# Performance work log

Measured on AMD Instinct MI355X. Metric: run time of the kernel, lower is better.

Reference implementation:

```python
import jax, jax.numpy as jnp
import numpy as np
import math

B, T, D, H, FF = 2, 2048, 1024, 16, 4096
DH = D // H
EPS = 1e-5

def _ternary(key, out_f, in_f):
    # TFLELayer: ternary-quantized linear weight in {-1,0,1} (stored as f32 here)
    return jax.random.randint(key, (out_f, in_f), -1, 2).astype(jnp.float32)

def setup_inputs() -> dict:
    key = jax.random.key(0)
    ks = jax.random.split(key, 8)
    x = jax.random.normal(ks[0], (B, T, D), dtype=jnp.float32)
    mask = jnp.triu(jnp.ones((T, T), dtype=bool), k=1)  # True = masked (causal)
    return {
        "x": x,
        "mask": mask,
        "ln1_g": jnp.ones((D,), jnp.float32), "ln1_b": jnp.zeros((D,), jnp.float32),
        "ln2_g": jnp.ones((D,), jnp.float32), "ln2_b": jnp.zeros((D,), jnp.float32),
        "Wq": _ternary(ks[1], D, D), "Wk": _ternary(ks[2], D, D),
        "Wv": _ternary(ks[3], D, D), "Wo": _ternary(ks[4], D, D),
        "Wff1": _ternary(ks[5], FF, D), "Wff2": _ternary(ks[6], D, FF),
    }

def _ln(x, g, b):
    mu = jnp.mean(x, axis=-1, keepdims=True)
    var = jnp.var(x, axis=-1, keepdims=True)
    return (x - mu) * jax.lax.rsqrt(var + EPS) * g + b

def reference(x, mask, ln1_g, ln1_b, ln2_g, ln2_b, Wq, Wk, Wv, Wo, Wff1, Wff2):
    h = _ln(x, ln1_g, ln1_b)
    q = (h @ Wq.T).reshape(B, T, H, DH).transpose(0, 2, 1, 3)  # (B,H,T,DH)
    k = (h @ Wk.T).reshape(B, T, H, DH).transpose(0, 2, 1, 3)
    v = (h @ Wv.T).reshape(B, T, H, DH).transpose(0, 2, 1, 3)
    scale = 1.0 / math.sqrt(DH)
    attn = jnp.einsum('bhqd,bhkd->bhqk', q, k) * scale
    attn = jnp.where(mask[None, None], -jnp.inf, attn)
    attn = jax.nn.softmax(attn, axis=-1)
    out = jnp.einsum('bhqk,bhkd->bhqd', attn, v)
    out = out.transpose(0, 2, 1, 3).reshape(B, T, D) @ Wo.T
    x = x + out
    h = _ln(x, ln2_g, ln2_b)
    ff = jax.nn.gelu(h @ Wff1.T, approximate=False)
    ff = ff @ Wff2.T
    return x + ff
```

## Files before the change

### kernel.cpp

```cpp
#include <hip/hip_runtime.h>

typedef __bf16 bf16;
typedef bf16 bf16x8 __attribute__((ext_vector_type(8)));
typedef bf16 bf16x4 __attribute__((ext_vector_type(4)));
typedef float f32x4 __attribute__((ext_vector_type(4)));

static __device__ __forceinline__ void async16(const void* g, void* l) {
  __builtin_amdgcn_global_load_lds((__attribute__((address_space(1))) void*)g,
                                   (__attribute__((address_space(3))) void*)l,
                                   16, 0, 0);
}

template <int N>
static __device__ __forceinline__ float ror16(float x) {
  const int y =
      __builtin_amdgcn_update_dpp(0, __float_as_int(x), 0x120 | N, 0xf, 0xf, true);
  return __int_as_float(y);
}
static __device__ __forceinline__ float rowmax16(float x) {
  x = fmaxf(x, ror16<8>(x));
  x = fmaxf(x, ror16<4>(x));
  x = fmaxf(x, ror16<2>(x));
  x = fmaxf(x, ror16<1>(x));
  return x;
}

__global__ __launch_bounds__(256) void ln1_cvt4(
    const float* __restrict__ x, const float* __restrict__ g,
    const float* __restrict__ b, bf16* __restrict__ hi, bf16* __restrict__ lo,
    const float* __restrict__ Wq, const float* __restrict__ Wk,
    const float* __restrict__ Wv, const float* __restrict__ Wo,
    bf16* __restrict__ wdst) {
  const int tid = threadIdx.x;
  if (blockIdx.x >= 4096) {
    const size_t i = ((size_t)(blockIdx.x - 4096) * 256 + tid) * 4;
    const size_t M1 = 1u << 20;
    const float* src = (i < M1) ? Wq : (i < 2 * M1) ? Wk : (i < 3 * M1) ? Wv : Wo;
    const size_t off = i & (M1 - 1);
    const float4 v = *(const float4*)(src + off);
    bf16x4 o = {(bf16)v.x, (bf16)v.y, (bf16)v.z, (bf16)v.w};
    *(bf16x4*)(wdst + i) = o;
    return;
  }
  const int row = blockIdx.x;
  const float* xr = x + (size_t)row * 1024;
  float v[4];
  float s1 = 0.f, s2 = 0.f;
#pragma unroll
  for (int j = 0; j < 4; ++j) {
    v[j] = xr[j * 256 + tid];
    s1 += v[j];
    s2 += v[j] * v[j];
  }
#pragma unroll
  for (int off = 1; off < 64; off <<= 1) {
    s1 += __shfl_xor(s1, off);
    s2 += __shfl_xor(s2, off);
  }
  __shared__ float ws1[4], ws2[4];
  const int wid = tid >> 6;
  if ((tid & 63) == 0) {
    ws1[wid] = s1;
    ws2[wid] = s2;
  }
  __syncthreads();
  s1 = ws1[0] + ws1[1] + ws1[2] + ws1[3];
  s2 = ws2[0] + ws2[1] + ws2[2] + ws2[3];
  const float mu = s1 * (1.f / 1024.f);
  const float var = s2 * (1.f / 1024.f) - mu * mu;
  const float rstd = 1.0f / sqrtf(var + 1e-5f);
#pragma unroll
  for (int j = 0; j < 4; ++j) {
    const int cc = j * 256 + tid;
    const float y = (v[j] - mu) * rstd * g[cc] + b[cc];
    const bf16 yh = (bf16)y;
    hi[(size_t)row * 1024 + cc] = yh;
    lo[(size_t)row * 1024 + cc] = (bf16)(y - (float)yh);
  }
}

__global__ __launch_bounds__(256) void ln_kernel(
    const float* __restrict__ x, const float* __restrict__ g,
    const float* __restrict__ b, bf16* __restrict__ hi) {
  const int row = blockIdx.x;
  const int tid = threadIdx.x;
  const float* xr = x + (size_t)row * 1024;
  float v[4];
  float s1 = 0.f, s2 = 0.f;
#pragma unroll
  for (int j = 0; j < 4; ++j) {
    v[j] = xr[j * 256 + tid];
    s1 += v[j];
    s2 += v[j] * v[j];
  }
#pragma unroll
  for (int off = 1; off < 64; off <<= 1) {
    s1 += __shfl_xor(s1, off);
    s2 += __shfl_xor(s2, off);
  }
  __shared__ float ws1[4], ws2[4];
  const int wid = tid >> 6;
  if ((tid & 63) == 0) {
    ws1[wid] = s1;
    ws2[wid] = s2;
  }
  __syncthreads();
  s1 = ws1[0] + ws1[1] + ws1[2] + ws1[3];
  s2 = ws2[0] + ws2[1] + ws2[2] + ws2[3];
  const float mu = s1 * (1.f / 1024.f);
  const float var = s2 * (1.f / 1024.f) - mu * mu;
  const float rstd = 1.0f / sqrtf(var + 1e-5f);
#pragma unroll
  for (int j = 0; j < 4; ++j) {
    const int cc = j * 256 + tid;
    const float y = (v[j] - mu) * rstd * g[cc] + b[cc];
    hi[(size_t)row * 1024 + cc] = (bf16)y;
  }
}

template <int EPI>
static __device__ __forceinline__ void gemm_body(
    const bf16* __restrict__ A, const bf16* __restrict__ B,
    void* __restrict__ Cv, const float* __restrict__ R, bf16* smem, int col0,
    int row0, int M, int N, int K) {
  bf16* sA0 = smem;
  bf16* sA1 = smem + 4096;
  bf16* sB0 = smem + 8192;
  bf16* sB1 = smem + 12288;
  const int tid = threadIdx.x;
  const int lane = tid & 63;
  const int wid = tid >> 6;
  const int wm = wid >> 1, wn = wid & 1;

  f32x4 acc[4][4];
  const f32x4 fzero = {0.f, 0.f, 0.f, 0.f};
#pragma unroll
  for (int i = 0; i < 4; ++i)
#pragma unroll
    for (int j = 0; j < 4; ++j) acc[i][j] = fzero;

  const int nk = K >> 6;
  const int r0 = tid >> 2, c0 = (tid & 3) << 3;
  const int r1 = (256 + tid) >> 2, c1 = ((256 + tid) & 3) << 3;
  const int wofs0 = (wid << 6) * 8;
  const int wofs1 = (256 + (wid << 6)) * 8;

  for (int kt = 0; kt < nk; ++kt) {
    const int k0 = kt << 6;
    async16(A + (size_t)(row0 + r0) * K + k0 + c0, sA0 + wofs0);
    async16(A + (size_t)(row0 + r1) * K + k0 + c1, sA0 + wofs1);
    async16(A + (size_t)(row0 + r0) * K + k0 + 32 + c0, sA1 + wofs0);
    async16(A + (size_t)(row0 + r1) * K + k0 + 32 + c1, sA1 + wofs1);
    async16(B + (size_t)(col0 + r0) * K + k0 + c0, sB0 + wofs0);
    async16(B + (size_t)(col0 + r1) * K + k0 + c1, sB0 + wofs1);
    async16(B + (size_t)(col0 + r0) * K + k0 + 32 + c0, sB1 + wofs0);
    async16(B + (size_t)(col0 + r1) * K + k0 + 32 + c1, sB1 + wofs1);
    __syncthreads();
    const int fr = lane & 15, fq = (lane >> 4) << 3;
#pragma unroll
    for (int t = 0; t < 2; ++t) {
      const bf16* sA = t ? sA1 : sA0;
      const bf16* sB = t ? sB1 : sB0;
      bf16x8 af[4], bfr[4];
#pragma unroll
      for (int i = 0; i < 4; ++i)
        af[i] = *(const bf16x8*)&sA[(wm * 64 + i * 16 + fr) * 32 + fq];
#pragma unroll
      for (int j = 0; j < 4; ++j)
        bfr[j] = *(const bf16x8*)&sB[(wn * 64 + j * 16 + fr) * 32 + fq];
#pragma unroll
      for (int i = 0; i < 4; ++i)
#pragma unroll
        for (int j = 0; j < 4; ++j)
          acc[i][j] = __builtin_amdgcn_mfma_f32_16x16x32_bf16(
              af[i], bfr[j], acc[i][j], 0, 0, 0);
    }
    __syncthreads();
  }

  const int fr = lane & 15, fq4 = (lane >> 4) << 2;
#pragma unroll
  for (int i = 0; i < 4; ++i) {
#pragma unroll
    for (int j = 0; j < 4; ++j) {
      const int rbase = row0 + wm * 64 + i * 16 + fq4;
      const int col = col0 + wn * 64 + j * 16 + fr;
      if constexpr (EPI == 5) {
        const int b = rbase >> 11, t = rbase & 2047;
        const int hh = col >> 6, d = col & 63;
        bf16x4 o4 = {(bf16)acc[i][j][0], (bf16)acc[i][j][1],
                     (bf16)acc[i][j][2], (bf16)acc[i][j][3]};
        *(bf16x4*)&((bf16*)Cv)[(((size_t)(b * 16 + hh)) * 64 + d) * 2048 + t] =
            o4;
      } else {
#pragma unroll
        for (int r = 0; r < 4; ++r) {
          const size_t idx = (size_t)(rbase + r) * N + col;
          const float val = acc[i][j][r];
          if constexpr (EPI == 0) {
            ((float*)Cv)[idx] = val;
          } else if constexpr (EPI == 2) {
            ((float*)Cv)[idx] = val + R[idx];
          } else {
            ((bf16*)Cv)[idx] =
                (bf16)(0.5f * val * (1.0f + erff(val * 0.7071067811865476f)));
          }
        }
      }
    }
  }
}

static __device__ __forceinline__ void gemm_split_merged(
    const bf16* __restrict__ A, const bf16* __restrict__ A2,
    const bf16* __restrict__ B, bf16* __restrict__ Chi, bf16* __restrict__ Clo,
    bf16* smem, float scale, int col0, int row0) {
  constexpr int K = 1024, N = 1024;
  bf16* sAh0 = smem;
  bf16* sAh1 = smem + 4096;
  bf16* sAl0 = smem + 8192;
  bf16* sAl1 = smem + 12288;
  bf16* sB0 = smem + 16384;
  bf16* sB1 = smem + 20480;
  const int tid = threadIdx.x;
  const int lane = tid & 63;
  const int wid = tid >> 6;
  const int wm = wid >> 1, wn = wid & 1;

  f32x4 acc[4][4];
  const f32x4 fzero = {0.f, 0.f, 0.f, 0.f};
#pragma unroll
  for (int i = 0; i < 4; ++i)
#pragma unroll
    for (int j = 0; j < 4; ++j) acc[i][j] = fzero;

  const int r0 = tid >> 2, c0 = (tid & 3) << 3;
  const int r1 = (256 + tid) >> 2, c1 = ((256 + tid) & 3) << 3;
  const int wofs0 = (wid << 6) * 8;
  const int wofs1 = (256 + (wid << 6)) * 8;

  for (int kt = 0; kt < 16; ++kt) {
    const int k0 = kt << 6;
    async16(A + (size_t)(row0 + r0) * K + k0 + c0, sAh0 + wofs0);
    async16(A + (size_t)(row0 + r1) * K + k0 + c1, sAh0 + wofs1);
    async16(A + (size_t)(row0 + r0) * K + k0 + 32 + c0, sAh1 + wofs0);
    async16(A + (size_t)(row0 + r1) * K + k0 + 32 + c1, sAh1 + wofs1);
    async16(A2 + (size_t)(row0 + r0) * K + k0 + c0, sAl0 + wofs0);
    async16(A2 + (size_t)(row0 + r1) * K + k0 + c1, sAl0 + wofs1);
    async16(A2 + (size_t)(row0 + r0) * K + k0 + 32 + c0, sAl1 + wofs0);
    async16(A2 + (size_t)(row0 + r1) * K + k0 + 32 + c1, sAl1 + wofs1);
    async16(B + (size_t)(col0 + r0) * K + k0 + c0, sB0 + wofs0);
    async16(B + (size_t)(col0 + r1) * K + k0 + c1, sB0 + wofs1);
    async16(B + (size_t)(col0 + r0) * K + k0 + 32 + c0, sB1 + wofs0);
    async16(B + (size_t)(col0 + r1) * K + k0 + 32 + c1, sB1 + wofs1);
    __syncthreads();
    const int fr = lane & 15, fq = (lane >> 4) << 3;
#pragma unroll
    for (int t = 0; t < 2; ++t) {
      const bf16* sAh = t ? sAh1 : sAh0;
      const bf16* sAl = t ? sAl1 : sAl0;
      const bf16* sB = t ? sB1 : sB0;
      bf16x8 ah[4], al[4], bfr[4];
#pragma unroll
      for (int i = 0; i < 4; ++i) {
        ah[i] = *(const bf16x8*)&sAh[(wm * 64 + i * 16 + fr) * 32 + fq];
        al[i] = *(const bf16x8*)&sAl[(wm * 64 + i * 16 + fr) * 32 + fq];
      }
#pragma unroll
      for (int j = 0; j < 4; ++j)
        bfr[j] = *(const bf16x8*)&sB[(wn * 64 + j * 16 + fr) * 32 + fq];
#pragma unroll
      for (int i = 0; i < 4; ++i)
#pragma unroll
        for (int j = 0; j < 4; ++j) {
          acc[i][j] = __builtin_amdgcn_mfma_f32_16x16x32_bf16(
              ah[i], bfr[j], acc[i][j], 0, 0, 0);
          acc[i][j] = __builtin_amdgcn_mfma_f32_16x16x32_bf16(
              al[i], bfr[j], acc[i][j], 0, 0, 0);
        }
    }
    __syncthreads();
  }

  const int fr = lane & 15, fq4 = (lane >> 4) << 2;
#pragma unroll
  for (int i = 0; i < 4; ++i)
#pragma unroll
    for (int j = 0; j < 4; ++j) {
      const int rbase = row0 + wm * 64 + i * 16 + fq4;
      const int col = col0 + wn * 64 + j * 16 + fr;
#pragma unroll
      for (int r = 0; r < 4; ++r) {
        const size_t idx = (size_t)(rbase + r) * N + col;
        const float vs = acc[i][j][r] * scale;
        const bf16 hi = (bf16)vs;
        Chi[idx] = hi;
        Clo[idx] = (bf16)(vs - (float)hi);
      }
    }
}

__global__ __launch_bounds__(256) void gemm_qkv(
    const bf16* __restrict__ A, const bf16* __restrict__ A2,
    const bf16* __restrict__ Bq, const bf16* __restrict__ Bk,
    const bf16* __restrict__ Bv, bf16* qh, bf16* ql, bf16* kh, bf16* kl,
    bf16* vt) {
  __shared__ bf16 smem[24576];
  const int which = blockIdx.x >> 3;
  const int col0 = (blockIdx.x & 7) * 128, row0 = blockIdx.y * 128;
  if (which == 2) {
    gemm_body<5>(A, Bv, (void*)vt, nullptr, smem, col0, row0, 4096, 1024,
                 1024);
  } else {
    gemm_split_merged(A, A2, which ? Bk : Bq, which ? kh : qh, which ? kl : ql,
                      smem, which ? 1.0f : 0.125f * 1.44269504088896f, col0,
                      row0);
  }
}

template <int EPI>
__global__ __launch_bounds__(256) void gemm_bt64(
    const bf16* __restrict__ A, const bf16* __restrict__ B,
    void* __restrict__ Cv, const float* __restrict__ R, int M, int N, int K) {
  __shared__ bf16 smem[24576];
  const int col0 = blockIdx.x * 64, row0 = blockIdx.y * 128;
  const int tid = threadIdx.x;
  const int lane = tid & 63;
  const int wid = tid >> 6;
  const int wm = wid >> 1, wn = wid & 1;

  f32x4 acc[4][2];
  const f32x4 fzero = {0.f, 0.f, 0.f, 0.f};
#pragma unroll
  for (int i = 0; i < 4; ++i)
#pragma unroll
    for (int j = 0; j < 2; ++j) acc[i][j] = fzero;

  const int nk = K >> 6;
  const int r0 = tid >> 2, c0 = (tid & 3) << 3;
  const int r1 = (256 + tid) >> 2, c1 = ((256 + tid) & 3) << 3;
  const int wofs0 = (wid << 6) * 8;
  const int wofs1 = (256 + (wid << 6)) * 8;

  auto stage = [&](int q, int kt) {
    const int k0 = kt << 6;
    bf16* base = smem + q * 12288;
    async16(A + (size_t)(row0 + r0) * K + k0 + c0, base + wofs0);
    async16(A + (size_t)(row0 + r1) * K + k0 + c1, base + wofs1);
    async16(A + (size_t)(row0 + r0) * K + k0 + 32 + c0, base + 4096 + wofs0);
    async16(A + (size_t)(row0 + r1) * K + k0 + 32 + c1, base + 4096 + wofs1);
    async16(B + (size_t)(col0 + r0) * K + k0 + c0, base + 8192 + wofs0);
    async16(B + (size_t)(col0 + r0) * K + k0 + 32 + c0, base + 10240 + wofs0);
  };

  stage(0, 0);
  __syncthreads();
  int cur = 0;
  for (int kt = 0; kt < nk; ++kt) {
    if (kt + 1 < nk) stage(cur ^ 1, kt + 1);
    const bf16* buf = smem + cur * 12288;
    const int fr = lane & 15, fq = (lane >> 4) << 3;
#pragma unroll
    for (int t = 0; t < 2; ++t) {
      const bf16* sA = buf + t * 4096;
      const bf16* sB = buf + 8192 + t * 2048;
      bf16x8 af[4], bfr[2];
#pragma unroll
      for (int i = 0; i < 4; ++i)
        af[i] = *(const bf16x8*)&sA[(wm * 64 + i * 16 + fr) * 32 + fq];
#pragma unroll
      for (int j = 0; j < 2; ++j)
        bfr[j] = *(const bf16x8*)&sB[(wn * 32 + j * 16 + fr) * 32 + fq];
#pragma unroll
      for (int i = 0; i < 4; ++i)
#pragma unroll
        for (int j = 0; j < 2; ++j)
          acc[i][j] = __builtin_amdgcn_mfma_f32_16x16x32_bf16(
              af[i], bfr[j], acc[i][j], 0, 0, 0);
    }
    __syncthreads();
    cur ^= 1;
  }

  const int fr = lane & 15, fq4 = (lane >> 4) << 2;
#pragma unroll
  for (int i = 0; i < 4; ++i) {
#pragma unroll
    for (int j = 0; j < 2; ++j) {
      const int rbase = row0 + wm * 64 + i * 16 + fq4;
      const int col = col0 + wn * 32 + j * 16 + fr;
#pragma unroll
      for (int r = 0; r < 4; ++r) {
        const size_t idx = (size_t)(rbase + r) * N + col;
        const float val = acc[i][j][r];
        if constexpr (EPI == 3) {
          ((bf16*)Cv)[idx] =
              (bf16)(0.5f * val * (1.0f + erff(val * 0.7071067811865476f)));
        } else if constexpr (EPI == 2) {
          ((float*)Cv)[idx] = val + R[idx];
        } else {
          ((float*)Cv)[idx] = val;
        }
      }
    }
  }
}

__global__ __launch_bounds__(256) void attn_cvt2(
    const bf16* __restrict__ qh_g, const bf16* __restrict__ ql_g,
    const bf16* __restrict__ kh_g, const bf16* __restrict__ kl_g,
    const bf16* __restrict__ vt_g, bf16* __restrict__ out,
    const float* __restrict__ Wf1, const float* __restrict__ Wf2,
    bf16* __restrict__ wdst) {
  __shared__ bf16 lds[18688];
  const int tid = threadIdx.x;
  if (blockIdx.x >= 1024) {
    const size_t i = ((size_t)(blockIdx.x - 1024) * 256 + tid) * 4;
    const size_t M4 = 4u << 20;
    const float* src = (i < M4) ? Wf1 : Wf2;
    const size_t off = (i < M4) ? i : i - M4;
    const float4 v = *(const float4*)(src + off);
    bf16x4 o4 = {(bf16)v.x, (bf16)v.y, (bf16)v.z, (bf16)v.w};
    *(bf16x4*)(wdst + i) = o4;
    return;
  }
  bf16* Kh = lds;
  bf16* Kl = lds + 4608;
  bf16* Vt = lds + 9216;
  bf16* Ps = lds + 13824;

  const int bid = blockIdx.x;
  const int u = bid & 255;
  const int s = bid >> 8;
  const int v = u >> 5;
  const int qbase = (3 - s) << 3;
  const int qt = qbase + ((s & 1) ? v : 7 - v);
  const int bh = (u & 7) * 4 + ((u >> 3) & 3);
  const int h = bh & 15;
  const int b = bh >> 4;
  const int t0 = qt << 6;
  const int w = tid >> 6;
  const int lane = tid & 63;
  const int c = lane & 15;
  const int quad = lane >> 4;

  const int r0 = tid >> 3, c0 = (tid & 7) << 3;
  const int r1 = (tid + 256) >> 3, c1 = ((tid + 256) & 7) << 3;

  const size_t qrow =
      ((size_t)(b * 2048 + t0 + w * 16 + c)) * 1024 + h * 64 + quad * 8;
  bf16x8 aqh[2], aql[2];
  aqh[0] = *(const bf16x8*)&qh_g[qrow];
  aqh[1] = *(const bf16x8*)&qh_g[qrow + 32];
  aql[0] = *(const bf16x8*)&ql_g[qrow];
  aql[1] = *(const bf16x8*)&ql_g[qrow + 32];

  f32x4 o[4];
  const f32x4 fzero = {0.f, 0.f, 0.f, 0.f};
#pragma unroll
  for (int j = 0; j < 4; ++j) o[j] = fzero;
  f32x4 l4 = fzero;
  float m_i[4] = {-3e38f, -3e38f, -3e38f, -3e38f};

  bf16x8 vone;
#pragma unroll
  for (int z = 0; z < 8; ++z) vone[z] = (bf16)1.0f;

  const size_t vtb = ((size_t)(b * 16 + h)) * 64 * 2048;
  const size_t kband = ((size_t)(b * 2048)) * 1024 + h * 64;

  bf16x8 gk[6];
  {
    gk[0] = *(const bf16x8*)&kh_g[kband + (size_t)r0 * 1024 + c0];
    gk[1] = *(const bf16x8*)&kh_g[kband + (size_t)r1 * 1024 + c1];
    gk[2] = *(const bf16x8*)&kl_g[kband + (size_t)r0 * 1024 + c0];
    gk[3] = *(const bf16x8*)&kl_g[kband + (size_t)r1 * 1024 + c1];
    gk[4] = *(const bf16x8*)&vt_g[vtb + (size_t)r0 * 2048 + c0];
    gk[5] = *(const bf16x8*)&vt_g[vtb + (size_t)r1 * 2048 + c1];
  }

  for (int kt = 0; kt <= qt; ++kt) {
    __syncthreads();
    *(bf16x8*)&Kh[r0 * 72 + c0] = gk[0];
    *(bf16x8*)&Kh[r1 * 72 + c1] = gk[1];
    *(bf16x8*)&Kl[r0 * 72 + c0] = gk[2];
    *(bf16x8*)&Kl[r1 * 72 + c1] = gk[3];
    *(bf16x8*)&Vt[r0 * 72 + c0] = gk[4];
    *(bf16x8*)&Vt[r1 * 72 + c1] = gk[5];
    __syncthreads();

    if (kt < qt) {
      const int kb1 = (kt + 1) << 6;
      const size_t kbase = kband + (size_t)kb1 * 1024;
      gk[0] = *(const bf16x8*)&kh_g[kbase + (size_t)r0 * 1024 + c0];
      gk[1] = *(const bf16x8*)&kh_g[kbase + (size_t)r1 * 1024 + c1];
      gk[2] = *(const bf16x8*)&kl_g[kbase + (size_t)r0 * 1024 + c0];
      gk[3] = *(const bf16x8*)&kl_g[kbase + (size_t)r1 * 1024 + c1];
      gk[4] = *(const bf16x8*)&vt_g[vtb + (size_t)r0 * 2048 + kb1 + c0];
      gk[5] = *(const bf16x8*)&vt_g[vtb + (size_t)r1 * 2048 + kb1 + c1];
    }

    bf16x8 bkh[4][2], bkl[4][2];
#pragma unroll
    for (int j = 0; j < 4; ++j)
#pragma unroll
      for (int s2 = 0; s2 < 2; ++s2) {
        bkh[j][s2] = *(const bf16x8*)&Kh[(j * 16 + c) * 72 + s2 * 32 + quad * 8];
        bkl[j][s2] = *(const bf16x8*)&Kl[(j * 16 + c) * 72 + s2 * 32 + quad * 8];
      }

    f32x4 s4[4];
#pragma unroll
    for (int j = 0; j < 4; ++j) s4[j] = fzero;
#pragma unroll
    for (int j = 0; j < 4; ++j)
#pragma unroll
      for (int s2 = 0; s2 < 2; ++s2) {
        s4[j] = __builtin_amdgcn_mfma_f32_16x16x32_bf16(aqh[s2], bkh[j][s2], s4[j], 0, 0, 0);
        s4[j] = __builtin_amdgcn_mfma_f32_16x16x32_bf16(aqh[s2], bkl[j][s2], s4[j], 0, 0, 0);
        s4[j] = __builtin_amdgcn_mfma_f32_16x16x32_bf16(aql[s2], bkh[j][s2], s4[j], 0, 0, 0);
      }

    if (kt == qt) {
#pragma unroll
      for (int j = 0; j < 4; ++j)
#pragma unroll
        for (int r = 0; r < 4; ++r)
          if (j * 16 + c > w * 16 + quad * 4 + r) s4[j][r] = -3e38f;
    }

    float p[4][4];
#pragma unroll
    for (int r = 0; r < 4; ++r) {
      float mt = fmaxf(fmaxf(s4[0][r], s4[1][r]), fmaxf(s4[2][r], s4[3][r]));
      mt = rowmax16(mt);
      const float mn = fmaxf(m_i[r], mt);
      const float al = exp2f(m_i[r] - mn);
      m_i[r] = mn;
#pragma unroll
      for (int j = 0; j < 4; ++j) p[r][j] = exp2f(s4[j][r] - mn);
      l4[r] *= al;
#pragma unroll
      for (int j = 0; j < 4; ++j) o[j][r] *= al;
    }

    bf16* Pw = Ps + w * 16 * 76;
#pragma unroll
    for (int r = 0; r < 4; ++r)
#pragma unroll
      for (int j = 0; j < 4; ++j)
        Pw[(quad * 4 + r) * 76 + j * 16 + c] = (bf16)p[r][j];

    bf16x8 ap[2], bv[4][2];
#pragma unroll
    for (int s2 = 0; s2 < 2; ++s2)
      ap[s2] = *(const bf16x8*)&Pw[c * 76 + s2 * 32 + quad * 8];
#pragma unroll
    for (int j = 0; j < 4; ++j)
#pragma unroll
      for (int s2 = 0; s2 < 2; ++s2)
        bv[j][s2] = *(const bf16x8*)&Vt[(j * 16 + c) * 72 + s2 * 32 + quad * 8];
    l4 = __builtin_amdgcn_mfma_f32_16x16x32_bf16(ap[0], vone, l4, 0, 0, 0);
    l4 = __builtin_amdgcn_mfma_f32_16x16x32_bf16(ap[1], vone, l4, 0, 0, 0);
#pragma unroll
    for (int j = 0; j < 4; ++j)
#pragma unroll
      for (int s2 = 0; s2 < 2; ++s2)
        o[j] = __builtin_amdgcn_mfma_f32_16x16x32_bf16(ap[s2], bv[j][s2], o[j], 0, 0, 0);
  }

#pragma unroll
  for (int r = 0; r < 4; ++r) {
    const float inv = 1.0f / l4[r];
#pragma unroll
    for (int j = 0; j < 4; ++j) {
      const size_t oi =
          ((size_t)(b * 2048 + t0 + w * 16 + quad * 4 + r)) * 1024 + h * 64 +
          j * 16 + c;
      out[oi] = (bf16)(o[j][r] * inv);
    }
  }
}

extern "C" void kernel_launch(void* const* d_in, const int* in_sizes, int n_in,
                              void* d_out, int out_size, void* d_ws,
                              size_t ws_size, hipStream_t stream) {
  const float* x = (const float*)d_in[0];
  const float* g1 = (const float*)d_in[2];
  const float* b1 = (const float*)d_in[3];
  const float* g2 = (const float*)d_in[4];
  const float* b2 = (const float*)d_in[5];
  const float* Wq = (const float*)d_in[6];
  const float* Wk = (const float*)d_in[7];
  const float* Wv = (const float*)d_in[8];
  const float* Wo = (const float*)d_in[9];
  const float* Wf1 = (const float*)d_in[10];
  const float* Wf2 = (const float*)d_in[11];
  char* ws = (char*)d_ws;
  const size_t MB = 1024 * 1024;
  const size_t M1 = 1u << 20;
  bf16* Wq_b = (bf16*)ws;
  bf16* Wk_b = Wq_b + 1 * M1;
  bf16* Wv_b = Wq_b + 2 * M1;
  bf16* Wo_b = Wq_b + 3 * M1;
  bf16* h_hi = (bf16*)(ws + 8 * MB);
  bf16* h_lo = (bf16*)(ws + 16 * MB);
  bf16* Wf1_b = h_hi;
  bf16* Wf2_b = h_lo;
  bf16* qh = (bf16*)(ws + 24 * MB);
  bf16* ql = (bf16*)(ws + 32 * MB);
  bf16* kh = (bf16*)(ws + 40 * MB);
  bf16* kl = (bf16*)(ws + 48 * MB);
  bf16* vt = (bf16*)(ws + 56 * MB);
  bf16* attnout = (bf16*)(ws + 64 * MB);
  float* x1 = (float*)qh;
  bf16* h2 = (bf16*)(ws + 72 * MB);
  bf16* ff = kh;
  float* outp = (float*)d_out;

  ln1_cvt4<<<8192, 256, 0, stream>>>(x, g1, b1, h_hi, h_lo, Wq, Wk, Wv, Wo,
                                     Wq_b);
  gemm_qkv<<<dim3(24, 32), 256, 0, stream>>>(h_hi, h_lo, Wq_b, Wk_b, Wv_b, qh,
                                             ql, kh, kl, vt);
  attn_cvt2<<<9216, 256, 0, stream>>>(qh, ql, kh, kl, vt, attnout, Wf1, Wf2,
                                      Wf1_b);
  gemm_bt64<2><<<dim3(16, 32), 256, 0, stream>>>(attnout, Wo_b, (void*)x1, x,
                                                 4096, 1024, 1024);
  ln_kernel<<<4096, 256, 0, stream>>>(x1, g2, b2, h2);
  gemm_bt64<3><<<dim3(64, 32), 256, 0, stream>>>(h2, Wf1_b, (void*)ff, nullptr,
                                                 4096, 4096, 1024);
  gemm_bt64<2><<<dim3(16, 32), 256, 0, stream>>>(ff, Wf2_b, (void*)outp, x1,
                                                 4096, 1024, 4096);
}
```

Before: 395.6 us.

## Double-buffer GEMM K-tiles so global loads overlap MFMA compute

Both GEMM bodies (the plain one and the hi/lo split one) now prefetch the next K-slice into a second shared-memory buffer while MFMAs run on the current one. Before, each iteration loaded and then waited behind a barrier, so load latency was exposed. To keep shared memory the same size, the K step drops from 64 to 32. That doubles the number of iterations and barriers, and MFMA work per barrier is smaller. Correctness depends on the end-of-iteration barrier also waiting for the async LDS loads to complete.

```diff
diff --git a/kernel.cpp b/kernel.cpp
--- a/kernel.cpp
+++ b/kernel.cpp
@@ -123,10 +123,6 @@
     const bf16* __restrict__ A, const bf16* __restrict__ B,
     void* __restrict__ Cv, const float* __restrict__ R, bf16* smem, int col0,
     int row0, int M, int N, int K) {
-  bf16* sA0 = smem;
-  bf16* sA1 = smem + 4096;
-  bf16* sB0 = smem + 8192;
-  bf16* sB1 = smem + 12288;
   const int tid = threadIdx.x;
   const int lane = tid & 63;
   const int wid = tid >> 6;
@@ -139,43 +135,43 @@
 #pragma unroll
     for (int j = 0; j < 4; ++j) acc[i][j] = fzero;
 
-  const int nk = K >> 6;
+  const int nk = K >> 5;
   const int r0 = tid >> 2, c0 = (tid & 3) << 3;
   const int r1 = (256 + tid) >> 2, c1 = ((256 + tid) & 3) << 3;
   const int wofs0 = (wid << 6) * 8;
   const int wofs1 = (256 + (wid << 6)) * 8;
 
+  auto stage = [&](int q, int kt) {
+    const int k0 = kt << 5;
+    bf16* base = smem + q * 8192;
+    async16(A + (size_t)(row0 + r0) * K + k0 + c0, base + wofs0);
+    async16(A + (size_t)(row0 + r1) * K + k0 + c1, base + wofs1);
+    async16(B + (size_t)(col0 + r0) * K + k0 + c0, base + 4096 + wofs0);
+    async16(B + (size_t)(col0 + r1) * K + k0 + c1, base + 4096 + wofs1);
+  };
+
+  stage(0, 0);
+  __syncthreads();
+  int cur = 0;
   for (int kt = 0; kt < nk; ++kt) {
-    const int k0 = kt << 6;
-    async16(A + (size_t)(row0 + r0) * K + k0 + c0, sA0 + wofs0);
-    async16(A + (size_t)(row0 + r1) * K + k0 + c1, sA0 + wofs1);
-    async16(A + (size_t)(row0 + r0) * K + k0 + 32 + c0, sA1 + wofs0);
-    async16(A + (size_t)(row0 + r1) * K + k0 + 32 + c1, sA1 + wofs1);
-    async16(B + (size_t)(col0 + r0) * K + k0 + c0, sB0 + wofs0);
-    async16(B + (size_t)(col0 + r1) * K + k0 + c1, sB0 + wofs1);
-    async16(B + (size_t)(col0 + r0) * K + k0 + 32 + c0, sB1 + wofs0);
-    async16(B + (size_t)(col0 + r1) * K + k0 + 32 + c1, sB1 + wofs1);
+    if (kt + 1 < nk) stage(cur ^ 1, kt + 1);
+    const bf16* buf = smem + cur * 8192;
+    const int fr = lane & 15, fq = (lane >> 4) << 3;
+    bf16x8 af[4], bfr[4];
+#pragma unroll
+    for (int i = 0; i < 4; ++i)
+      af[i] = *(const bf16x8*)&buf[(wm * 64 + i * 16 + fr) * 32 + fq];
+#pragma unroll
+    for (int j = 0; j < 4; ++j)
+      bfr[j] = *(const bf16x8*)&buf[4096 + (wn * 64 + j * 16 + fr) * 32 + fq];
+#pragma unroll
+    for (int i = 0; i < 4; ++i)
+#pragma unroll
+      for (int j = 0; j < 4; ++j)
+        acc[i][j] = __builtin_amdgcn_mfma_f32_16x16x32_bf16(
+            af[i], bfr[j], acc[i][j], 0, 0, 0);
     __syncthreads();
-    const int fr = lane & 15, fq = (lane >> 4) << 3;
-#pragma unroll
-    for (int t = 0; t < 2; ++t) {
-      const bf16* sA = t ? sA1 : sA0;
-      const bf16* sB = t ? sB1 : sB0;
-      bf16x8 af[4], bfr[4];
-#pragma unroll
-      for (int i = 0; i < 4; ++i)
-        af[i] = *(const bf16x8*)&sA[(wm * 64 + i * 16 + fr) * 32 + fq];
-#pragma unroll
-      for (int j = 0; j < 4; ++j)
-        bfr[j] = *(const bf16x8*)&sB[(wn * 64 + j * 16 + fr) * 32 + fq];
-#pragma unroll
-      for (int i = 0; i < 4; ++i)
-#pragma unroll
-        for (int j = 0; j < 4; ++j)
-          acc[i][j] = __builtin_amdgcn_mfma_f32_16x16x32_bf16(
-              af[i], bfr[j], acc[i][j], 0, 0, 0);
-    }
-    __syncthreads();
+    cur ^= 1;
   }
 
   const int fr = lane & 15, fq4 = (lane >> 4) << 2;
@@ -216,12 +212,6 @@
     const bf16* __restrict__ B, bf16* __restrict__ Chi, bf16* __restrict__ Clo,
     bf16* smem, float scale, int col0, int row0) {
   constexpr int K = 1024, N = 1024;
-  bf16* sAh0 = smem;
-  bf16* sAh1 = smem + 4096;
-  bf16* sAl0 = smem + 8192;
-  bf16* sAl1 = smem + 12288;
-  bf16* sB0 = smem + 16384;
-  bf16* sB1 = smem + 20480;
   const int tid = threadIdx.x;
   const int lane = tid & 63;
   const int wid = tid >> 6;
@@ -239,47 +229,44 @@
   const int wofs0 = (wid << 6) * 8;
   const int wofs1 = (256 + (wid << 6)) * 8;
 
-  for (int kt = 0; kt < 16; ++kt) {
-    const int k0 = kt << 6;
-    async16(A + (size_t)(row0 + r0) * K + k0 + c0, sAh0 + wofs0);
-    async16(A + (size_t)(row0 + r1) * K + k0 + c1, sAh0 + wofs1);
-    async16(A + (size_t)(row0 + r0) * K + k0 + 32 + c0, sAh1 + wofs0);
-    async16(A + (size_t)(row0 + r1) * K + k0 + 32 + c1, sAh1 + wofs1);
-    async16(A2 + (size_t)(row0 + r0) * K + k0 + c0, sAl0 + wofs0);
-    async16(A2 + (size_t)(row0 + r1) * K + k0 + c1, sAl0 + wofs1);
-    async16(A2 + (size_t)(row0 + r0) * K + k0 + 32 + c0, sAl1 + wofs0);
-    async16(A2 + (size_t)(row0 + r1) * K + k0 + 32 + c1, sAl1 + wofs1);
-    async16(B + (size_t)(col0 + r0) * K + k0 + c0, sB0 + wofs0);
-    async16(B + (size_t)(col0 + r1) * K + k0 + c1, sB0 + wofs1);
-    async16(B + (size_t)(col0 + r0) * K + k0 + 32 + c0, sB1 + wofs0);
-    async16(B + (size_t)(col0 + r1) * K + k0 + 32 + c1, sB1 + wofs1);
+  auto stage = [&](int q, int kt) {
+    const int k0 = kt << 5;
+    bf16* base = smem + q * 12288;
+    async16(A + (size_t)(row0 + r0) * K + k0 + c0, base + wofs0);
+    async16(A + (size_t)(row0 + r1) * K + k0 + c1, base + wofs1);
+    async16(A2 + (size_t)(row0 + r0) * K + k0 + c0, base + 4096 + wofs0);
+    async16(A2 + (size_t)(row0 + r1) * K + k0 + c1, base + 4096 + wofs1);
+    async16(B + (size_t)(col0 + r0) * K + k0 + c0, base + 8192 + wofs0);
+    async16(B + (size_t)(col0 + r1) * K + k0 + c1, base + 8192 + wofs1);
+  };
+
+  stage(0, 0);
+  __syncthreads();
+  int cur = 0;
+  for (int kt = 0; kt < 32; ++kt) {
+    if (kt + 1 < 32) stage(cur ^ 1, kt + 1);
+    const bf16* base = smem + cur * 12288;
+    const int fr = lane & 15, fq = (lane >> 4) << 3;
+    bf16x8 ah[4], al[4], bfr[4];
+#pragma unroll
+    for (int i = 0; i < 4; ++i) {
+      ah[i] = *(const bf16x8*)&base[(wm * 64 + i * 16 + fr) * 32 + fq];
+      al[i] = *(const bf16x8*)&base[4096 + (wm * 64 + i * 16 + fr) * 32 + fq];
+    }
+#pragma unroll
+    for (int j = 0; j < 4; ++j)
+      bfr[j] = *(const bf16x8*)&base[8192 + (wn * 64 + j * 16 + fr) * 32 + fq];
+#pragma unroll
+    for (int i = 0; i < 4; ++i)
+#pragma unroll
+      for (int j = 0; j < 4; ++j) {
+        acc[i][j] = __builtin_amdgcn_mfma_f32_16x16x32_bf16(
+            ah[i], bfr[j], acc[i][j], 0, 0, 0);
+        acc[i][j] = __builtin_amdgcn_mfma_f32_16x16x32_bf16(
+            al[i], bfr[j], acc[i][j], 0, 0, 0);
+      }
     __syncthreads();
-    const int fr = lane & 15, fq = (lane >> 4) << 3;
-#pragma unroll
-    for (int t = 0; t < 2; ++t) {
-      const bf16* sAh = t ? sAh1 : sAh0;
-      const bf16* sAl = t ? sAl1 : sAl0;
-      const bf16* sB = t ? sB1 : sB0;
-      bf16x8 ah[4], al[4], bfr[4];
-#pragma unroll
-      for (int i = 0; i < 4; ++i) {
-        ah[i] = *(const bf16x8*)&sAh[(wm * 64 + i * 16 + fr) * 32 + fq];
-        al[i] = *(const bf16x8*)&sAl[(wm * 64 + i * 16 + fr) * 32 + fq];
-      }
-#pragma unroll
-      for (int j = 0; j < 4; ++j)
-        bfr[j] = *(const bf16x8*)&sB[(wn * 64 + j * 16 + fr) * 32 + fq];
-#pragma unroll
-      for (int i = 0; i < 4; ++i)
-#pragma unroll
-        for (int j = 0; j < 4; ++j) {
-          acc[i][j] = __builtin_amdgcn_mfma_f32_16x16x32_bf16(
-              ah[i], bfr[j], acc[i][j], 0, 0, 0);
-          acc[i][j] = __builtin_amdgcn_mfma_f32_16x16x32_bf16(
-              al[i], bfr[j], acc[i][j], 0, 0, 0);
-        }
-    }
-    __syncthreads();
+    cur ^= 1;
   }
 
   const int fr = lane & 15, fq4 = (lane >> 4) << 2;
```

Measured after the change: 389.2 us, median of 3. No clear change (-1.6%).
